# Kernel tuning notes

Hardware: AMD Instinct MI355X
Metric: run time of the kernel (lower is better)

## Reference

```python
import jax, jax.numpy as jnp
import numpy as np

G = 128                      # grid_size
THRESHOLD_RATIO = 1000.0
BOUNDS = (0.0, 4.5, 0.5, 5.5)  # default grid_bounds (x_min, x_max, y_min, y_max)


def setup_inputs() -> dict:
    key = jax.random.key(0)
    k1, k2, k3 = jax.random.split(key, 3)
    B, N = 8, 524288
    y_pred = jax.random.normal(k1, (B, N, 2), dtype=jnp.float32)
    y_true = jax.random.normal(k2, (B, N, 2), dtype=jnp.float32)
    u = jax.random.uniform(k3, (B, N, 3), dtype=jnp.float32)
    x_min, x_max, y_min, y_max = BOUNDS
    coords = jnp.stack([
        x_min + u[..., 0] * (x_max - x_min),
        y_min + u[..., 1] * (y_max - y_min),
        u[..., 2],
    ], axis=-1)
    return {"y_pred": y_pred, "y_true": y_true, "coords": coords}


def _mean3x3(x, pad_mode):
    # x: [C, G, G] -> 3x3 box filter; 'edge' = replicate pad, 'zero' = constant pad
    xp = jnp.pad(x, ((0, 0), (1, 1), (1, 1)), mode=pad_mode)
    kernel = jnp.full((1, 1, 3, 3), 1.0 / 9.0, dtype=x.dtype)
    return jax.lax.conv_general_dilated(xp[:, None], kernel, (1, 1), 'VALID')[:, 0]


def _scatter_to_grid(coords, vals):
    # coords: [N, 3]; vals: [4, N] (pred_r, pred_i, true_r, true_i) -> [4, G, G]
    x_min, x_max, y_min, y_max = BOUNDS
    xn = (coords[:, 0] - x_min) / (x_max - x_min) * (G - 1)
    yn = (coords[:, 1] - y_min) / (y_max - y_min) * (G - 1)
    xi = jnp.clip(jnp.round(xn).astype(jnp.int32), 0, G - 1)
    yi = jnp.clip(jnp.round(yn).astype(jnp.int32), 0, G - 1)
    flat = yi * G + xi  # [N]
    field = jnp.zeros((4, G * G), vals.dtype).at[:, flat].add(vals)
    count = jnp.zeros((G * G,), vals.dtype).at[flat].add(1.0)
    field = jnp.where(count > 0, field / count, field)
    field = field.reshape(4, G, G)
    count = count.reshape(G, G)
    # 3 iterations of hole-filling (where is a no-op when no cell is empty,
    # matching the torch data-dependent branch exactly)
    for _ in range(3):
        sm = _mean3x3(field, 'edge')
        field = jnp.where(count == 0, sm, field)
        csm = _mean3x3(count[None], 'constant')[0]
        count = jnp.where((count == 0) & (csm > 0), 1.0, count)
    return field


def reference(y_pred, y_true, coords):
    # stack the 4 scalar fields so one scatter pass per sample handles all of them
    vals = jnp.stack([y_pred[..., 0], y_pred[..., 1],
                      y_true[..., 0], y_true[..., 1]], axis=1)  # [B, 4, N]
    grids = jax.vmap(_scatter_to_grid)(coords, vals)  # [B, 4, G, G]
    x_min, x_max, y_min, y_max = BOUNDS
    dx = (x_max - x_min) / (G - 1)
    dy = (y_max - y_min) / (G - 1)
    pred_c = jax.lax.complex(grids[:, 0], grids[:, 1])
    true_c = jax.lax.complex(grids[:, 2], grids[:, 3])
    scale = dx * dy
    fft_pred = jnp.fft.fftshift(jnp.fft.fft2(pred_c), axes=(-2, -1)) * scale
    fft_true = jnp.fft.fftshift(jnp.fft.fft2(true_c), axes=(-2, -1)) * scale
    fa = jnp.abs(fft_true)                               # [B, G, G]
    famax = fa.max(axis=(-2, -1), keepdims=True)
    mask = (fa >= famax / THRESHOLD_RATIO).astype(fa.dtype)
    weight = fa ** 2 / (famax ** 2 + 1e-10)
    d = (fft_pred - fft_true) * mask
    weighted_diff = (jnp.abs(d) ** 2) * weight
    per_sample = weighted_diff.sum(axis=(-2, -1)) / (mask.sum(axis=(-2, -1)) + 1e-10)
    return per_sample.mean()
```

## Files before the change

### kernel.cpp

```cpp
#include <hip/hip_runtime.h>
#include <hip/hip_fp16.h>
#include <math.h>

#define BB 8
#define NPTS 524288
#define G 128
#define GG (G*G)
#define SWORDS 40960

#define OFF_FIELD 0
#define OFF_COUNT (BB*4*GG)
#define OFF_FAMAX (OFF_COUNT + BB*GG)
#define OFF_FLAG  (OFF_FAMAX + 8)
#define OFF_T     (OFF_FAMAX + 24)
#define OFF_Y     (OFF_T + BB*2*GG*2)
#define OFF_STAGE (OFF_T)

__device__ __forceinline__ unsigned pack_h2(float x, float y) {
    __half2 h = __floats2half2_rn(x, y);
    return *(unsigned*)&h;
}

__global__ __launch_bounds__(1024) void k_scatter_sort(const float4* __restrict__ co4,
                                                       const float4* __restrict__ yp4,
                                                       const float4* __restrict__ yt4,
                                                       unsigned* __restrict__ stage,
                                                       unsigned* __restrict__ flags) {
    extern __shared__ unsigned sm[];
    unsigned* cnt = sm;
    unsigned long long* data = (unsigned long long*)(sm + 8192);
    unsigned* dscr = sm + 8192;

    const int t = threadIdx.x;
    const int blk = blockIdx.x;
    const unsigned qbase = (unsigned)blk * 4096u;

    if (blk == 0 && t < 8) flags[t] = 0u;

    for (int k = t; k < 8192; k += 1024) cnt[k] = 0u;
    __syncthreads();

    unsigned cr[16];
#pragma unroll
    for (int g = 0; g < 4; g++) {
        unsigned qa = qbase + (unsigned)(g * 1024 + t);
        float4 A = co4[3u * qa], B = co4[3u * qa + 1], C = co4[3u * qa + 2];
        float cx[4], cy[4];
        cx[0] = A.x; cy[0] = A.y; cx[1] = A.w; cy[1] = B.x;
        cx[2] = B.z; cy[2] = B.w; cx[3] = C.y; cy[3] = C.z;
#pragma unroll
        for (int j = 0; j < 4; j++) {
            float xn = (cx[j] - 0.0f) / 4.5f * 127.0f;
            float yn = (cy[j] - 0.5f) / 5.0f * 127.0f;
            int xi = min(max((int)rintf(xn), 0), G - 1);
            int yi = min(max((int)rintf(yn), 0), G - 1);
            unsigned cell = (unsigned)(yi * G + xi);
            unsigned sh = (cell & 1u) * 16u;
            unsigned old = atomicAdd(&cnt[cell >> 1], 1u << sh);
            unsigned rank = (old >> sh) & 0xFFFFu;
            cr[g * 4 + j] = cell | (rank << 16);
        }
    }
    __syncthreads();

    unsigned w[8], ssum = 0;
#pragma unroll
    for (int j = 0; j < 8; j++) {
        w[j] = cnt[8 * t + j];
        ssum += (w[j] & 0xFFFFu) + (w[j] >> 16);
    }
    unsigned lane = (unsigned)t & 63u, wid = (unsigned)t >> 6;
    unsigned inc = ssum;
    for (int off = 1; off < 64; off <<= 1) {
        unsigned v = __shfl_up(inc, off);
        if (lane >= (unsigned)off) inc += v;
    }
    if (lane == 63u) dscr[wid] = inc;
    __syncthreads();
    unsigned wbase = 0;
#pragma unroll
    for (int k = 0; k < 16; k++) {
        unsigned v = dscr[k];
        if ((unsigned)k < wid) wbase += v;
    }
    unsigned ex = wbase + inc - ssum;
#pragma unroll
    for (int j = 0; j < 8; j++) {
        unsigned c0 = w[j] & 0xFFFFu, c1 = w[j] >> 16;
        cnt[8 * t + j] = ex | ((ex + c0) << 16);
        ex += c0 + c1;
    }
    __syncthreads();

    const unsigned short* off16 = (const unsigned short*)cnt;
#pragma unroll
    for (int g = 0; g < 4; g++) {
        unsigned qa = qbase + (unsigned)(g * 1024 + t);
        float4 P0 = yp4[2u * qa], P1 = yp4[2u * qa + 1];
        float4 Q0 = yt4[2u * qa], Q1 = yt4[2u * qa + 1];
        unsigned pv[4], tv[4];
        pv[0] = pack_h2(P0.x, P0.y); pv[1] = pack_h2(P0.z, P0.w);
        pv[2] = pack_h2(P1.x, P1.y); pv[3] = pack_h2(P1.z, P1.w);
        tv[0] = pack_h2(Q0.x, Q0.y); tv[1] = pack_h2(Q0.z, Q0.w);
        tv[2] = pack_h2(Q1.x, Q1.y); tv[3] = pack_h2(Q1.z, Q1.w);
#pragma unroll
        for (int j = 0; j < 4; j++) {
            unsigned c = cr[g * 4 + j] & 0xFFFFu;
            unsigned rank = cr[g * 4 + j] >> 16;
            unsigned pos = (unsigned)off16[c] + rank;
            data[pos] = ((unsigned long long)tv[j] << 32) | (unsigned long long)pv[j];
        }
    }
    __syncthreads();

    unsigned* sb = stage + (size_t)blk * SWORDS;
    unsigned o[17];
#pragma unroll
    for (int j = 0; j < 8; j++) {
        unsigned wv = cnt[8 * t + j];
        o[2 * j] = wv & 0xFFFFu;
        o[2 * j + 1] = wv >> 16;
    }
    o[16] = (t == 1023) ? 16384u : (unsigned)off16[16 * (t + 1)];
    unsigned pvw[16], tvw[16];
#pragma unroll
    for (int k = 0; k < 16; k++) {
        float pr = 0.f, pi = 0.f, tr = 0.f, ti = 0.f;
        for (unsigned j = o[k]; j < o[k + 1]; j++) {
            unsigned long long d = data[j];
            unsigned lo = (unsigned)d, hi = (unsigned)(d >> 32);
            float2 fp = __half22float2(*(__half2*)&lo);
            float2 ft = __half22float2(*(__half2*)&hi);
            pr += fp.x; pi += fp.y; tr += ft.x; ti += ft.y;
        }
        pvw[k] = pack_h2(pr, pi);
        tvw[k] = pack_h2(tr, ti);
    }
#pragma unroll
    for (int j = 0; j < 4; j++)
        *(uint4*)(sb + 16 * t + 4 * j) = make_uint4(pvw[4*j], pvw[4*j+1], pvw[4*j+2], pvw[4*j+3]);
#pragma unroll
    for (int j = 0; j < 4; j++)
        *(uint4*)(sb + 16384 + 16 * t + 4 * j) = make_uint4(tvw[4*j], tvw[4*j+1], tvw[4*j+2], tvw[4*j+3]);
#pragma unroll
    for (int j = 0; j < 8; j++) {
        float ce = (float)(o[2 * j + 1] - o[2 * j]);
        float cd = (float)(o[2 * j + 2] - o[2 * j + 1]);
        sb[32768 + 8 * t + j] = pack_h2(ce, cd);
    }
}

__global__ __launch_bounds__(1024) void k_scatter(const float4* __restrict__ co4,
                                                  const float4* __restrict__ yp4,
                                                  const float4* __restrict__ yt4,
                                                  unsigned* __restrict__ stage,
                                                  unsigned* __restrict__ flags,
                                                  int rep) {
    extern __shared__ unsigned sm[];
    int blk = blockIdx.x;
    int r = blk % rep;
    int b = blk / rep;
    if (blk == 0 && threadIdx.x < 8) flags[threadIdx.x] = 0u;
    for (int k = threadIdx.x; k < SWORDS / 4; k += 1024)
        ((uint4*)sm)[k] = make_uint4(0u, 0u, 0u, 0u);
    __syncthreads();
    unsigned ldsbase = (unsigned)(uintptr_t)sm;
    int ppb = NPTS / rep;
    int nq = ppb >> 2;
    size_t qbase = ((size_t)b * NPTS + (size_t)r * ppb) >> 2;
#define DOPT(cx, cy, vx, vy, wx, wy) do {                                   \
        float xn = ((cx) - 0.0f) / 4.5f * 127.0f;                           \
        float yn = ((cy) - 0.5f) / 5.0f * 127.0f;                           \
        int xi = min(max((int)rintf(xn), 0), G - 1);                        \
        int yi = min(max((int)rintf(yn), 0), G - 1);                        \
        unsigned cell = (unsigned)(yi * G + xi);                            \
        unsigned av = ldsbase + cell * 4u;                                  \
        asm volatile("ds_pk_add_f16 %0, %1" :: "v"(av), "v"(pack_h2(vx, vy))); \
        asm volatile("ds_pk_add_f16 %0, %1" :: "v"(av + 65536u), "v"(pack_h2(wx, wy))); \
        unsigned ac = ldsbase + 131072u + (cell >> 1) * 4u;                 \
        unsigned cw = (cell & 1u) ? 0x3C000000u : 0x00003C00u;              \
        asm volatile("ds_pk_add_f16 %0, %1" :: "v"(ac), "v"(cw));           \
    } while (0)
    for (int q = threadIdx.x; q < nq; q += 2048) {
        size_t qa = qbase + q, qb = qa + 1024;
        float4 A0 = co4[3 * qa], B0 = co4[3 * qa + 1], C0 = co4[3 * qa + 2];
        float4 P00 = yp4[2 * qa], P01 = yp4[2 * qa + 1];
        float4 Q00 = yt4[2 * qa], Q01 = yt4[2 * qa + 1];
        float4 A1 = co4[3 * qb], B1 = co4[3 * qb + 1], C1 = co4[3 * qb + 2];
        float4 P10 = yp4[2 * qb], P11 = yp4[2 * qb + 1];
        float4 Q10 = yt4[2 * qb], Q11 = yt4[2 * qb + 1];
        DOPT(A0.x, A0.y, P00.x, P00.y, Q00.x, Q00.y);
        DOPT(A0.w, B0.x, P00.z, P00.w, Q00.z, Q00.w);
        DOPT(B0.z, B0.w, P01.x, P01.y, Q01.x, Q01.y);
        DOPT(C0.y, C0.z, P01.z, P01.w, Q01.z, Q01.w);
        DOPT(A1.x, A1.y, P10.x, P10.y, Q10.x, Q10.y);
        DOPT(A1.w, B1.x, P10.z, P10.w, Q10.z, Q10.w);
        DOPT(B1.z, B1.w, P11.x, P11.y, Q11.x, Q11.y);
        DOPT(C1.y, C1.z, P11.z, P11.w, Q11.z, Q11.w);
    }
#undef DOPT
    asm volatile("s_waitcnt lgkmcnt(0)" ::: "memory");
    __syncthreads();
    unsigned* sb = stage + (size_t)blk * SWORDS;
    for (int k = threadIdx.x * 4; k < SWORDS; k += 4096)
        *(uint4*)(sb + k) = *(const uint4*)(sm + k);
}

__global__ __launch_bounds__(256) void k_reduce(const unsigned* __restrict__ stage,
                                                float* __restrict__ field,
                                                float* __restrict__ cnt,
                                                unsigned* __restrict__ famax,
                                                unsigned* __restrict__ flags,
                                                float* __restrict__ out,
                                                int rep) {
    if (blockIdx.x == 0) {
        if (threadIdx.x < 8) famax[threadIdx.x] = 0u;
        if (threadIdx.x == 8) out[0] = 0.f;
    }
    int idx = blockIdx.x * 256 + threadIdx.x;
    int k = idx & 8191;
    int b = idx >> 13;
    const unsigned* sb = stage + (size_t)b * rep * SWORDS;
    float p0r = 0, p0i = 0, p1r = 0, p1i = 0;
    float t0r = 0, t0i = 0, t1r = 0, t1i = 0;
    float n0 = 0, n1 = 0;
    for (int r = 0; r < rep; r++) {
        const unsigned* pp = sb + (size_t)r * SWORDS;
        uint2 pv = *(const uint2*)(pp + 2 * k);
        uint2 tv = *(const uint2*)(pp + 16384 + 2 * k);
        unsigned cw = pp[32768 + k];
        float2 f;
        f = __half22float2(*(__half2*)&pv.x); p0r += f.x; p0i += f.y;
        f = __half22float2(*(__half2*)&pv.y); p1r += f.x; p1i += f.y;
        f = __half22float2(*(__half2*)&tv.x); t0r += f.x; t0i += f.y;
        f = __half22float2(*(__half2*)&tv.y); t1r += f.x; t1i += f.y;
        f = __half22float2(*(__half2*)&cw);   n0  += f.x; n1  += f.y;
    }
    int hole = (n0 == 0.f) || (n1 == 0.f);
    if (__any(hole)) {
        if ((threadIdx.x & 63) == 0) atomicOr(&flags[b], 1u);
    }
    if (n0 > 0.f) { p0r /= n0; p0i /= n0; t0r /= n0; t0i /= n0; }
    if (n1 > 0.f) { p1r /= n1; p1i /= n1; t1r /= n1; t1i /= n1; }
    float2* f2 = (float2*)field;
    size_t o = (size_t)b * 4 * (GG / 2) + k;
    f2[o]                = make_float2(p0r, p1r);
    f2[o + (GG / 2)]     = make_float2(p0i, p1i);
    f2[o + 2 * (GG / 2)] = make_float2(t0r, t1r);
    f2[o + 3 * (GG / 2)] = make_float2(t0i, t1i);
    ((float2*)cnt)[(size_t)b * (GG / 2) + k] = make_float2(n0, n1);
}

__global__ __launch_bounds__(1024) void k_holefill(float* __restrict__ field,
                                                   const float* __restrict__ cnt,
                                                   const unsigned* __restrict__ flags) {
    int b = blockIdx.x >> 2, ch = blockIdx.x & 3;
    if (flags[b] == 0u) return;
    extern __shared__ float smf[];
    float* fs = smf;
    float* cs = smf + GG;
    float* fg = field + ((size_t)b * 4 + ch) * GG;
    const float* cg = cnt + (size_t)b * GG;
    int tid = threadIdx.x;
    for (int k = 0; k < 16; k++) {
        int cell = tid + k * 1024;
        cs[cell] = cg[cell];
        fs[cell] = fg[cell];
    }
    __syncthreads();
    float nf[16], nc[16];
    for (int it = 0; it < 3; ++it) {
        for (int k = 0; k < 16; k++) {
            int cell = tid + k * 1024;
            int y = cell >> 7, x = cell & 127;
            float c = cs[cell];
            float f = fs[cell];
            if (c == 0.f) {
                float s9 = 0.f;
                for (int dy = -1; dy <= 1; dy++)
                    for (int dx = -1; dx <= 1; dx++) {
                        int yy = min(max(y + dy, 0), G - 1);
                        int xx = min(max(x + dx, 0), G - 1);
                        s9 += fs[yy * G + xx];
                    }
                f = s9 * (1.0f / 9.0f);
                float c9 = 0.f;
                for (int dy = -1; dy <= 1; dy++)
                    for (int dx = -1; dx <= 1; dx++) {
                        int yy = y + dy, xx = x + dx;
                        if (yy >= 0 && yy < G && xx >= 0 && xx < G) c9 += cs[yy * G + xx];
                    }
                if (c9 > 0.f) c = 1.0f;
            }
            nf[k] = f; nc[k] = c;
        }
        __syncthreads();
        for (int k = 0; k < 16; k++) {
            int cell = tid + k * 1024;
            fs[cell] = nf[k];
            cs[cell] = nc[k];
        }
        __syncthreads();
    }
    for (int k = 0; k < 16; k++) {
        int cell = tid + k * 1024;
        fg[cell] = fs[cell];
    }
}

template <int PASS>
__global__ __launch_bounds__(256) void k_dft(const float* __restrict__ in,
                                             float* __restrict__ out,
                                             unsigned* __restrict__ famax) {
    __shared__ float2 xs[8][128];
    int blk = blockIdx.x;
    int rc = blk & 15;
    int bf = blk >> 4;
    int tid = threadIdx.x;
    if (PASS == 0) {
        const float* re = in + ((size_t)(bf >> 1) * 4 + (size_t)(bf & 1) * 2) * GG + rc * 8 * G;
        const float* im = re + GG;
        for (int e = 0; e < 4; e++) {
            int idx = tid + e * 256;
            xs[idx >> 7][idx & 127] = make_float2(re[idx], im[idx]);
        }
    } else {
        const float2* cx = (const float2*)in + (size_t)bf * GG + rc * 8 * G;
        for (int e = 0; e < 4; e++) {
            int idx = tid + e * 256;
            xs[idx >> 7][idx & 127] = cx[idx];
        }
    }
    __syncthreads();

    int rloc = (tid >> 6) * 2;
    int kk = tid & 63;
    float ang = -3.14159265358979323846f / 64.0f * (float)kk;
    float si, sr;
    sincosf(ang, &si, &sr);

    float e0r = 0.f, e0i = 0.f, o0r = 0.f, o0i = 0.f;
    float e1r = 0.f, e1i = 0.f, o1r = 0.f, o1i = 0.f;
    float tr = 1.f, ti = 0.f;
#pragma unroll 8
    for (int n = 0; n < 128; n += 2) {
        float2 x0 = xs[rloc][n];
        float2 x1 = xs[rloc + 1][n];
        e0r += x0.x * tr - x0.y * ti;  e0i += x0.x * ti + x0.y * tr;
        e1r += x1.x * tr - x1.y * ti;  e1i += x1.x * ti + x1.y * tr;
        float t2r = tr * sr - ti * si, t2i = tr * si + ti * sr;
        x0 = xs[rloc][n + 1];
        x1 = xs[rloc + 1][n + 1];
        o0r += x0.x * t2r - x0.y * t2i;  o0i += x0.x * t2i + x0.y * t2r;
        o1r += x1.x * t2r - x1.y * t2i;  o1i += x1.x * t2i + x1.y * t2r;
        tr = t2r * sr - t2i * si;  ti = t2r * si + t2i * sr;
    }

    float2 a00 = make_float2(e0r + o0r, e0i + o0i);
    float2 a01 = make_float2(e1r + o1r, e1i + o1i);
    float2 a10 = make_float2(e0r - o0r, e0i - o0i);
    float2 a11 = make_float2(e1r - o1r, e1i - o1i);

    float2* ob = (float2*)out + (size_t)bf * GG;
    int r0 = rc * 8 + rloc;
    ob[kk * G + r0]            = a00;
    ob[kk * G + r0 + 1]        = a01;
    ob[(kk + 64) * G + r0]     = a10;
    ob[(kk + 64) * G + r0 + 1] = a11;

    if (PASS == 1 && (bf & 1)) {
        float m = fmaxf(fmaxf(sqrtf(a00.x * a00.x + a00.y * a00.y),
                              sqrtf(a01.x * a01.x + a01.y * a01.y)),
                        fmaxf(sqrtf(a10.x * a10.x + a10.y * a10.y),
                              sqrtf(a11.x * a11.x + a11.y * a11.y)));
        for (int off = 32; off; off >>= 1) m = fmaxf(m, __shfl_down(m, off));
        if ((tid & 63) == 0) atomicMax(&famax[bf >> 1], __float_as_uint(m));
    }
}

__global__ __launch_bounds__(1024) void k_loss(const float* __restrict__ Ybuf,
                                               const unsigned* __restrict__ famax,
                                               float* __restrict__ out) {
    int b = blockIdx.x;
    const float2* Yp = (const float2*)Ybuf + (size_t)(b * 2 + 0) * GG;
    const float2* Yt = (const float2*)Ybuf + (size_t)(b * 2 + 1) * GG;
    const float s = (4.5f / 127.0f) * (5.0f / 127.0f);
    float fam = __uint_as_float(famax[b]) * s;
    float fam2 = fam * fam + 1e-10f;
    float thr = fam / 1000.0f;
    float swd = 0.f, smask = 0.f;
    for (int k = 0; k < 16; k++) {
        int idx = threadIdx.x + k * 1024;
        float2 p = Yp[idx], t = Yt[idx];
        float pr = p.x * s, pi = p.y * s;
        float qr = t.x * s, qi = t.y * s;
        float fa = sqrtf(qr * qr + qi * qi);
        if (fa >= thr) {
            float w = fa * fa / fam2;
            float dr = pr - qr, di = pi - qi;
            swd += (dr * dr + di * di) * w;
            smask += 1.f;
        }
    }
    for (int off = 32; off; off >>= 1) {
        swd += __shfl_down(swd, off);
        smask += __shfl_down(smask, off);
    }
    __shared__ float rs[16], rm[16];
    int wid = threadIdx.x >> 6, lane = threadIdx.x & 63;
    if (lane == 0) { rs[wid] = swd; rm[wid] = smask; }
    __syncthreads();
    if (threadIdx.x == 0) {
        float a = 0.f, m = 0.f;
        for (int w = 0; w < 16; w++) { a += rs[w]; m += rm[w]; }
        atomicAdd(out, (a / (m + 1e-10f)) * 0.125f);
    }
}

extern "C" void kernel_launch(void* const* d_in, const int* in_sizes, int n_in,
                              void* d_out, int out_size, void* d_ws, size_t ws_size,
                              hipStream_t stream) {
    const float* yp = (const float*)d_in[0];
    const float* yt = (const float*)d_in[1];
    const float* co = (const float*)d_in[2];
    float* ws = (float*)d_ws;
    float* field = ws + OFF_FIELD;
    float* cnt   = ws + OFF_COUNT;
    unsigned* famax = (unsigned*)(ws + OFF_FAMAX);
    unsigned* flags = (unsigned*)(ws + OFF_FLAG);
    float* T = ws + OFF_T;
    float* Y = ws + OFF_Y;
    unsigned* stage = (unsigned*)(ws + OFF_STAGE);

    int rep = 32;
    while (rep > 1 &&
           ((size_t)OFF_T + (size_t)BB * rep * SWORDS) * 4 > ws_size)
        rep >>= 1;

    if (rep == 32) {
        k_scatter_sort<<<BB * 32, 1024, SWORDS * sizeof(unsigned), stream>>>(
            (const float4*)co, (const float4*)yp, (const float4*)yt, stage, flags);
    } else {
        k_scatter<<<BB * rep, 1024, SWORDS * sizeof(unsigned), stream>>>(
            (const float4*)co, (const float4*)yp, (const float4*)yt, stage, flags, rep);
    }
    k_reduce<<<BB * (GG / 2) / 256, 256, 0, stream>>>(
        stage, field, cnt, famax, flags, (float*)d_out, rep);
    k_holefill<<<BB * 4, 1024, 2 * GG * sizeof(float), stream>>>(field, cnt, flags);
    k_dft<0><<<BB * 2 * 16, 256, 0, stream>>>(field, T, famax);
    k_dft<1><<<BB * 2 * 16, 256, 0, stream>>>(T, Y, famax);
    k_loss<<<BB, 1024, 0, stream>>>(Y, famax, (float*)d_out);
}
```

Measured before the change: 91.08 us.

## Fuse hole-filling into first DFT pass with halo rows; templatize reduce rep

Removes the separate hole-fill kernel. Each first-pass DFT block now loads its 8 rows plus a 3-row halo of field and count, runs the 3 fill iterations locally in shared memory when the sample's hole flag is set, and then transforms. Dropping that kernel saves a launch and a full-field round trip through global memory, and the fill work is spread over 256 blocks instead of 32. The cost is redundant halo loads and computation across blocks. The reduce kernel also becomes a template on the replication count so its accumulation loop can be fully unrolled for the common case.

```diff
diff --git a/kernel.cpp b/kernel.cpp
--- a/kernel.cpp
+++ b/kernel.cpp
@@ -206,13 +206,14 @@
         *(uint4*)(sb + k) = *(const uint4*)(sm + k);
 }
 
+template <int REP>
 __global__ __launch_bounds__(256) void k_reduce(const unsigned* __restrict__ stage,
                                                 float* __restrict__ field,
                                                 float* __restrict__ cnt,
                                                 unsigned* __restrict__ famax,
                                                 unsigned* __restrict__ flags,
                                                 float* __restrict__ out,
-                                                int rep) {
+                                                int rep_rt) {
     if (blockIdx.x == 0) {
         if (threadIdx.x < 8) famax[threadIdx.x] = 0u;
         if (threadIdx.x == 8) out[0] = 0.f;
@@ -220,10 +221,12 @@
     int idx = blockIdx.x * 256 + threadIdx.x;
     int k = idx & 8191;
     int b = idx >> 13;
+    const int rep = (REP > 0) ? REP : rep_rt;
     const unsigned* sb = stage + (size_t)b * rep * SWORDS;
     float p0r = 0, p0i = 0, p1r = 0, p1i = 0;
     float t0r = 0, t0i = 0, t1r = 0, t1i = 0;
     float n0 = 0, n1 = 0;
+#pragma unroll
     for (int r = 0; r < rep; r++) {
         const unsigned* pp = sb + (size_t)r * SWORDS;
         uint2 pv = *(const uint2*)(pp + 2 * k);
@@ -251,84 +254,80 @@
     ((float2*)cnt)[(size_t)b * (GG / 2) + k] = make_float2(n0, n1);
 }
 
-__global__ __launch_bounds__(1024) void k_holefill(float* __restrict__ field,
-                                                   const float* __restrict__ cnt,
-                                                   const unsigned* __restrict__ flags) {
-    int b = blockIdx.x >> 2, ch = blockIdx.x & 3;
-    if (flags[b] == 0u) return;
-    extern __shared__ float smf[];
-    float* fs = smf;
-    float* cs = smf + GG;
-    float* fg = field + ((size_t)b * 4 + ch) * GG;
-    const float* cg = cnt + (size_t)b * GG;
-    int tid = threadIdx.x;
-    for (int k = 0; k < 16; k++) {
-        int cell = tid + k * 1024;
-        cs[cell] = cg[cell];
-        fs[cell] = fg[cell];
-    }
-    __syncthreads();
-    float nf[16], nc[16];
-    for (int it = 0; it < 3; ++it) {
-        for (int k = 0; k < 16; k++) {
-            int cell = tid + k * 1024;
-            int y = cell >> 7, x = cell & 127;
-            float c = cs[cell];
-            float f = fs[cell];
-            if (c == 0.f) {
-                float s9 = 0.f;
-                for (int dy = -1; dy <= 1; dy++)
-                    for (int dx = -1; dx <= 1; dx++) {
-                        int yy = min(max(y + dy, 0), G - 1);
-                        int xx = min(max(x + dx, 0), G - 1);
-                        s9 += fs[yy * G + xx];
-                    }
-                f = s9 * (1.0f / 9.0f);
-                float c9 = 0.f;
-                for (int dy = -1; dy <= 1; dy++)
-                    for (int dx = -1; dx <= 1; dx++) {
-                        int yy = y + dy, xx = x + dx;
-                        if (yy >= 0 && yy < G && xx >= 0 && xx < G) c9 += cs[yy * G + xx];
-                    }
-                if (c9 > 0.f) c = 1.0f;
-            }
-            nf[k] = f; nc[k] = c;
-        }
-        __syncthreads();
-        for (int k = 0; k < 16; k++) {
-            int cell = tid + k * 1024;
-            fs[cell] = nf[k];
-            cs[cell] = nc[k];
-        }
-        __syncthreads();
-    }
-    for (int k = 0; k < 16; k++) {
-        int cell = tid + k * 1024;
-        fg[cell] = fs[cell];
-    }
-}
-
-template <int PASS>
-__global__ __launch_bounds__(256) void k_dft(const float* __restrict__ in,
-                                             float* __restrict__ out,
-                                             unsigned* __restrict__ famax) {
+__global__ __launch_bounds__(256) void k_dft0(const float* __restrict__ field,
+                                              const float* __restrict__ cnt,
+                                              const unsigned* __restrict__ flags,
+                                              float* __restrict__ out) {
     __shared__ float2 xs[8][128];
+    __shared__ float hre[14 * 128], him[14 * 128], hcn[14 * 128];
     int blk = blockIdx.x;
     int rc = blk & 15;
     int bf = blk >> 4;
+    int b = bf >> 1;
     int tid = threadIdx.x;
-    if (PASS == 0) {
-        const float* re = in + ((size_t)(bf >> 1) * 4 + (size_t)(bf & 1) * 2) * GG + rc * 8 * G;
-        const float* im = re + GG;
+    const float* re = field + ((size_t)b * 4 + (size_t)(bf & 1) * 2) * GG;
+    const float* im = re + GG;
+    int r0 = rc * 8;
+
+    if (flags[b] == 0u) {
         for (int e = 0; e < 4; e++) {
             int idx = tid + e * 256;
-            xs[idx >> 7][idx & 127] = make_float2(re[idx], im[idx]);
+            xs[idx >> 7][idx & 127] = make_float2(re[r0 * G + idx], im[r0 * G + idx]);
         }
     } else {
-        const float2* cx = (const float2*)in + (size_t)bf * GG + rc * 8 * G;
+        const float* cg = cnt + (size_t)b * GG;
+        for (int k = 0; k < 7; k++) {
+            int c = tid + k * 256;
+            int s = c >> 7, x = c & 127;
+            int gr = r0 - 3 + s;
+            if (gr >= 0 && gr < G) {
+                hre[c] = re[gr * G + x];
+                him[c] = im[gr * G + x];
+                hcn[c] = cg[gr * G + x];
+            } else {
+                hre[c] = 0.f; him[c] = 0.f; hcn[c] = 1.f;
+            }
+        }
+        __syncthreads();
+        for (int it = 0; it < 3; ++it) {
+            float nr[7], ni[7], nc[7];
+            int lo = r0 - 2 + it, hi = r0 + 9 - it;
+            for (int k = 0; k < 7; k++) {
+                int c = tid + k * 256;
+                int s = c >> 7, x = c & 127;
+                int gr = r0 - 3 + s;
+                float cv = hcn[c], fr = hre[c], fi = him[c];
+                if (gr >= max(lo, 0) && gr <= min(hi, G - 1) && cv == 0.f) {
+                    float sr = 0.f, si2 = 0.f, sc = 0.f;
+                    for (int dy = -1; dy <= 1; dy++)
+                        for (int dx = -1; dx <= 1; dx++) {
+                            int yy = min(max(gr + dy, 0), G - 1);
+                            int xx = min(max(x + dx, 0), G - 1);
+                            int sidx = (yy - (r0 - 3)) * G + xx;
+                            sr += hre[sidx];
+                            si2 += him[sidx];
+                            int ry = gr + dy, rx = x + dx;
+                            if (ry >= 0 && ry < G && rx >= 0 && rx < G)
+                                sc += hcn[(ry - (r0 - 3)) * G + rx];
+                        }
+                    fr = sr * (1.0f / 9.0f);
+                    fi = si2 * (1.0f / 9.0f);
+                    if (sc > 0.f) cv = 1.0f;
+                }
+                nr[k] = fr; ni[k] = fi; nc[k] = cv;
+            }
+            __syncthreads();
+            for (int k = 0; k < 7; k++) {
+                int c = tid + k * 256;
+                hre[c] = nr[k]; him[c] = ni[k]; hcn[c] = nc[k];
+            }
+            __syncthreads();
+        }
         for (int e = 0; e < 4; e++) {
             int idx = tid + e * 256;
-            xs[idx >> 7][idx & 127] = cx[idx];
+            int row = idx >> 7, x = idx & 127;
+            int c = (row + 3) * G + x;
+            xs[row][x] = make_float2(hre[c], him[c]);
         }
     }
     __syncthreads();
@@ -356,6 +355,52 @@
         tr = t2r * sr - t2i * si;  ti = t2r * si + t2i * sr;
     }
 
+    float2* ob = (float2*)out + (size_t)bf * GG;
+    int orow = r0 + rloc;
+    ob[kk * G + orow]            = make_float2(e0r + o0r, e0i + o0i);
+    ob[kk * G + orow + 1]        = make_float2(e1r + o1r, e1i + o1i);
+    ob[(kk + 64) * G + orow]     = make_float2(e0r - o0r, e0i - o0i);
+    ob[(kk + 64) * G + orow + 1] = make_float2(e1r - o1r, e1i - o1i);
+}
+
+__global__ __launch_bounds__(256) void k_dft1(const float* __restrict__ in,
+                                              float* __restrict__ out,
+                                              unsigned* __restrict__ famax) {
+    __shared__ float2 xs[8][128];
+    int blk = blockIdx.x;
+    int rc = blk & 15;
+    int bf = blk >> 4;
+    int tid = threadIdx.x;
+    const float2* cx = (const float2*)in + (size_t)bf * GG + rc * 8 * G;
+    for (int e = 0; e < 4; e++) {
+        int idx = tid + e * 256;
+        xs[idx >> 7][idx & 127] = cx[idx];
+    }
+    __syncthreads();
+
+    int rloc = (tid >> 6) * 2;
+    int kk = tid & 63;
+    float ang = -3.14159265358979323846f / 64.0f * (float)kk;
+    float si, sr;
+    sincosf(ang, &si, &sr);
+
+    float e0r = 0.f, e0i = 0.f, o0r = 0.f, o0i = 0.f;
+    float e1r = 0.f, e1i = 0.f, o1r = 0.f, o1i = 0.f;
+    float tr = 1.f, ti = 0.f;
+#pragma unroll 8
+    for (int n = 0; n < 128; n += 2) {
+        float2 x0 = xs[rloc][n];
+        float2 x1 = xs[rloc + 1][n];
+        e0r += x0.x * tr - x0.y * ti;  e0i += x0.x * ti + x0.y * tr;
+        e1r += x1.x * tr - x1.y * ti;  e1i += x1.x * ti + x1.y * tr;
+        float t2r = tr * sr - ti * si, t2i = tr * si + ti * sr;
+        x0 = xs[rloc][n + 1];
+        x1 = xs[rloc + 1][n + 1];
+        o0r += x0.x * t2r - x0.y * t2i;  o0i += x0.x * t2i + x0.y * t2r;
+        o1r += x1.x * t2r - x1.y * t2i;  o1i += x1.x * t2i + x1.y * t2r;
+        tr = t2r * sr - t2i * si;  ti = t2r * si + t2i * sr;
+    }
+
     float2 a00 = make_float2(e0r + o0r, e0i + o0i);
     float2 a01 = make_float2(e1r + o1r, e1i + o1i);
     float2 a10 = make_float2(e0r - o0r, e0i - o0i);
@@ -368,7 +413,7 @@
     ob[(kk + 64) * G + r0]     = a10;
     ob[(kk + 64) * G + r0 + 1] = a11;
 
-    if (PASS == 1 && (bf & 1)) {
+    if (bf & 1) {
         float m = fmaxf(fmaxf(sqrtf(a00.x * a00.x + a00.y * a00.y),
                               sqrtf(a01.x * a01.x + a01.y * a01.y)),
                         fmaxf(sqrtf(a10.x * a10.x + a10.y * a10.y),
@@ -440,14 +485,15 @@
     if (rep == 32) {
         k_scatter_sort<<<BB * 32, 1024, SWORDS * sizeof(unsigned), stream>>>(
             (const float4*)co, (const float4*)yp, (const float4*)yt, stage, flags);
+        k_reduce<32><<<BB * (GG / 2) / 256, 256, 0, stream>>>(
+            stage, field, cnt, famax, flags, (float*)d_out, 32);
     } else {
         k_scatter<<<BB * rep, 1024, SWORDS * sizeof(unsigned), stream>>>(
             (const float4*)co, (const float4*)yp, (const float4*)yt, stage, flags, rep);
-    }
-    k_reduce<<<BB * (GG / 2) / 256, 256, 0, stream>>>(
-        stage, field, cnt, famax, flags, (float*)d_out, rep);
-    k_holefill<<<BB * 4, 1024, 2 * GG * sizeof(float), stream>>>(field, cnt, flags);
-    k_dft<0><<<BB * 2 * 16, 256, 0, stream>>>(field, T, famax);
-    k_dft<1><<<BB * 2 * 16, 256, 0, stream>>>(T, Y, famax);
+        k_reduce<0><<<BB * (GG / 2) / 256, 256, 0, stream>>>(
+            stage, field, cnt, famax, flags, (float*)d_out, rep);
+    }
+    k_dft0<<<BB * 2 * 16, 256, 0, stream>>>(field, cnt, flags, T);
+    k_dft1<<<BB * 2 * 16, 256, 0, stream>>>(T, Y, famax);
     k_loss<<<BB, 1024, 0, stream>>>(Y, famax, (float*)d_out);
 }
```

After: 85.59 us. 1.06x faster.
